# Kernel optimization log

Hardware: AMD Instinct MI355X
Metric: run time of the kernel (lower is better)

The kernel has to match this reference:

```python
import jax, jax.numpy as jnp
import numpy as np

N_NODES = 50000
N_EDGES = 800000
D = 128
N_REL = 237


def _layer(x, W_I, W_O, rel, b, src, dst):
    # messages over real edges: compose (sub) then project
    msg = (x[src] - rel[edge_safe(dst, None) if False else None] if False else (x[src] - rel_gather)) if False else None
    # (see clean version below)
    raise NotImplementedError


def compgcn_layer(x, W_I, W_O, rel, b, src, dst, etype):
    n = x.shape[0]
    # real edges: gather, compose (sub), project, scatter-add at dst
    msg = (x[src] - rel[etype]) @ W_I.T            # [E, out]
    aggr = jax.ops.segment_sum(msg, dst, num_segments=n)
    # self loops (added with edge_type 0): each node contributes to itself
    self_msg = (x - rel[0]) @ W_I.T                # [N, out]
    # update: aggregated messages + W_O(x) + bias
    return aggr + self_msg + x @ W_O.T + b


def setup_inputs() -> dict:
    key = jax.random.key(0)
    ks = jax.random.split(key, 12)
    x = jax.random.normal(ks[0], (N_NODES, D), dtype=jnp.float32)
    edge_index = jax.random.randint(ks[1], (2, N_EDGES), 0, N_NODES, dtype=jnp.int32)
    edge_type = jax.random.randint(ks[2], (N_EDGES,), 0, N_REL, dtype=jnp.int32)
    def xavier(k, shape):
        bound = float(np.sqrt(6.0 / (shape[0] + shape[1])))
        return jax.random.uniform(k, shape, jnp.float32, -bound, bound)
    return {
        "x": x,
        "edge_index": edge_index,
        "edge_type": edge_type,
        "W_I1": xavier(ks[3], (D, D)), "W_O1": xavier(ks[4], (D, D)),
        "rel1": xavier(ks[5], (N_REL, D)), "b1": jnp.zeros((D,), jnp.float32),
        "W_I2": xavier(ks[6], (D, D)), "W_O2": xavier(ks[7], (D, D)),
        "rel2": xavier(ks[8], (N_REL, D)), "b2": jnp.zeros((D,), jnp.float32),
    }


def reference(x, edge_index, edge_type, W_I1, W_O1, rel1, b1, W_I2, W_O2, rel2, b2):
    src, dst = edge_index[0], edge_index[1]
    h = compgcn_layer(x, W_I1, W_O1, rel1, b1, src, dst, edge_type)
    h = jax.nn.relu(h)  # dropout inactive in eval
    out = compgcn_layer(h, W_I2, W_O2, rel2, b2, src, dst, edge_type)
    return out
```

## Files before the change

### kernel.cpp

```cpp
#include <hip/hip_runtime.h>

#define D 128
#define CAP 3072

typedef __attribute__((ext_vector_type(8))) short short8;
typedef __attribute__((ext_vector_type(4))) float f32x4;

__device__ __forceinline__ float blo(unsigned w) { return __uint_as_float(w << 16); }
__device__ __forceinline__ float bhi(unsigned w) { return __uint_as_float(w & 0xFFFF0000u); }
__device__ __forceinline__ unsigned bpack(float a, float b) {
    unsigned ua = __float_as_uint(a), ub = __float_as_uint(b);
    ua += 0x7FFFu + ((ua >> 16) & 1u);
    ub += 0x7FFFu + ((ub >> 16) & 1u);
    return (ua >> 16) | (ub & 0xFFFF0000u);
}

__global__ __launch_bounds__(256) void setup_mega(
    const float* __restrict__ x,
    const int* __restrict__ srcA, const int* __restrict__ dstA,
    const int* __restrict__ etA,
    const float* __restrict__ WI1, const float* __restrict__ WO1,
    const float* __restrict__ WI2, const float* __restrict__ WO2,
    const float* __restrict__ rel1, const float* __restrict__ rel2,
    const float* __restrict__ b1, const float* __restrict__ b2,
    unsigned* __restrict__ A1,
    unsigned* __restrict__ Wt1, unsigned* __restrict__ Wt2,
    float* __restrict__ c1, float* __restrict__ c2,
    unsigned* __restrict__ rb1, unsigned* __restrict__ rb2,
    int* __restrict__ coarseCnt, unsigned* __restrict__ bulk,
    int N, int E, int relHalf, int nCoarse) {
    int tid = threadIdx.x;
    int bx = blockIdx.x;
    const int B1B = (E + 1023) / 1024;

    if (bx < B1B) {
        __shared__ unsigned pay[1024];
        __shared__ unsigned short ck[1024];
        __shared__ int hist[400];
        __shared__ int base[400];
        int e0 = bx * 1024;
        int cnt = E - e0; if (cnt > 1024) cnt = 1024;
        for (int i = tid; i < nCoarse; i += 256) hist[i] = 0;
        __syncthreads();
        for (int i = tid; i < cnt; i += 256) {
            int e = e0 + i;
            int d = dstA[e];
            pay[i] = (unsigned)srcA[e] | ((unsigned)etA[e] << 17) | ((unsigned)(d & 127) << 25);
            int c = d >> 7;
            ck[i] = (unsigned short)c;
            atomicAdd(&hist[c], 1);
        }
        __syncthreads();
        for (int i = tid; i < nCoarse; i += 256) {
            int h = hist[i];
            base[i] = (h > 0) ? (i * CAP + atomicAdd(&coarseCnt[i], h)) : 0;
            hist[i] = 0;
        }
        __syncthreads();
        for (int i = tid; i < cnt; i += 256) {
            int c = ck[i];
            int pos = base[c] + atomicAdd(&hist[c], 1);
            bulk[pos] = pay[i];
        }
        return;
    }
    bx -= B1B;
    const int CB = (N * 32 + 255) / 256;
    if (bx < CB) {
        int idx = bx * 256 + tid;
        if (idx < N * 32) {
            int n = idx >> 5, q = idx & 31;
            float4 v = ((const float4*)x)[idx];
            uint2 o;
            o.x = bpack(v.x, v.y);
            o.y = bpack(v.z, v.w);
            *(uint2*)(A1 + (size_t)n * 128 + 64 + q * 2) = o;
        }
        return;
    }
    bx -= CB;
    if (bx < 128) {
        int layer = bx >> 6;
        const float* WI = layer ? WI2 : WI1;
        const float* WO = layer ? WO2 : WO1;
        unsigned* Wt = layer ? Wt2 : Wt1;
        int idx = (bx & 63) * 256 + tid;
        int j = idx >> 7;
        int kk = idx & 127;
        int k0 = kk * 2;
        float a, b;
        if (k0 < D) {
            a = WI[j * D + k0];
            b = WI[j * D + k0 + 1];
        } else {
            int kx = k0 - D;
            a = WI[j * D + kx]     + WO[j * D + kx];
            b = WI[j * D + kx + 1] + WO[j * D + kx + 1];
        }
        Wt[idx] = bpack(a, b);
        return;
    }
    bx -= 128;
    if (bx == 0) {
        int layer = tid >> 7;
        int j = tid & (D - 1);
        const float* WI = layer ? WI2 : WI1;
        const float* b  = layer ? b2  : b1;
        const float* rl = layer ? rel2 : rel1;
        float s = b[j];
        for (int k = 0; k < D; ++k) s = fmaf(-WI[j * D + k], rl[k], s);
        (layer ? c2 : c1)[j] = s;
        return;
    }
    bx -= 1;
    {
        int idx = bx * 256 + tid;
        if (idx < 2 * relHalf) {
            const float* src = (idx < relHalf) ? rel1 : rel2;
            unsigned* dst = (idx < relHalf) ? rb1 : rb2;
            int k = (idx < relHalf) ? idx : idx - relHalf;
            float4 v = ((const float4*)src)[k];
            uint2 o;
            o.x = bpack(v.x, v.y);
            o.y = bpack(v.z, v.w);
            *(uint2*)(dst + (size_t)k * 2) = o;
        }
    }
}

__global__ __launch_bounds__(512) void scan_coarse(const int* __restrict__ coarseCnt,
                                                   int* __restrict__ coarseBase,
                                                   int nCoarse, int E) {
    __shared__ int arr[512];
    int tid = threadIdx.x;
    int c = (tid < nCoarse) ? coarseCnt[tid] : 0;
    arr[tid] = c;
    __syncthreads();
    for (int off = 1; off < 512; off <<= 1) {
        int v = (tid >= off) ? arr[tid - off] : 0;
        __syncthreads();
        arr[tid] += v;
        __syncthreads();
    }
    if (tid < nCoarse) coarseBase[tid] = arr[tid] - c;
    if (tid == nCoarse) coarseBase[tid] = E;
}

__global__ __launch_bounds__(256) void bucket2(const unsigned* __restrict__ bulk,
                                               const int* __restrict__ coarseCnt,
                                               const int* __restrict__ coarseBase,
                                               int* __restrict__ row_ptr,
                                               int* __restrict__ col,
                                               int N, int E, int nCoarse) {
    __shared__ unsigned pay[CAP];
    __shared__ int hist[128];
    __shared__ int cur[128];
    int c = blockIdx.x;
    int tid = threadIdx.x;
    int cnt = coarseCnt[c];
    int cb  = coarseBase[c];
    const unsigned* seg = bulk + (size_t)c * CAP;
    if (tid < 128) hist[tid] = 0;
    __syncthreads();
    for (int i = tid; i < cnt; i += 256) {
        unsigned v = seg[i];
        pay[i] = v;
        atomicAdd(&hist[v >> 25], 1);
    }
    __syncthreads();
    int f = tid;
    int myCnt = (f < 128) ? hist[f] : 0;
    for (int off = 1; off < 128; off <<= 1) {
        int v = (f < 128 && f >= off) ? hist[f - off] : 0;
        __syncthreads();
        if (f < 128) hist[f] += v;
        __syncthreads();
    }
    if (f < 128) {
        int excl = hist[f] - myCnt;
        int d = (c << 7) + f;
        if (d < N) row_ptr[d] = cb + excl;
        cur[f] = cb + excl;
    }
    if (c == nCoarse - 1 && tid == 0) row_ptr[N] = E;
    __syncthreads();
    for (int i = tid; i < cnt; i += 256) {
        unsigned v = pay[i];
        int pos = atomicAdd(&cur[v >> 25], 1);
        col[pos] = (int)(v & 0x1FFFFFFu);
    }
}

__global__ __launch_bounds__(256) void gather_kernel(const unsigned* __restrict__ Asrc,
                                                     const int* __restrict__ col,
                                                     const int* __restrict__ row_ptr,
                                                     const unsigned* __restrict__ relb,
                                                     unsigned* __restrict__ Adst, int N) {
    int n = blockIdx.x * 8 + (threadIdx.x >> 5);
    if (n >= N) return;
    int lane = threadIdx.x & 31;
    int beg = row_ptr[n];
    int end = row_ptr[n + 1];
    float4 s = make_float4(0.f, 0.f, 0.f, 0.f);
    int e = beg;
    for (; e + 11 < end; e += 12) {
        uint2 u[12], r[12];
#pragma unroll
        for (int t = 0; t < 12; ++t) {
            int c = col[e + t];
            u[t] = *(const uint2*)(Asrc + (size_t)(c & 0x1FFFF) * 128 + 64 + 2 * lane);
            r[t] = *(const uint2*)(relb + (size_t)(c >> 17) * 64 + 2 * lane);
        }
#pragma unroll
        for (int t = 0; t < 12; ++t) {
            s.x += blo(u[t].x) - blo(r[t].x);
            s.y += bhi(u[t].x) - bhi(r[t].x);
            s.z += blo(u[t].y) - blo(r[t].y);
            s.w += bhi(u[t].y) - bhi(r[t].y);
        }
    }
    for (; e + 3 < end; e += 4) {
        uint2 u[4], r[4];
#pragma unroll
        for (int t = 0; t < 4; ++t) {
            int c = col[e + t];
            u[t] = *(const uint2*)(Asrc + (size_t)(c & 0x1FFFF) * 128 + 64 + 2 * lane);
            r[t] = *(const uint2*)(relb + (size_t)(c >> 17) * 64 + 2 * lane);
        }
#pragma unroll
        for (int t = 0; t < 4; ++t) {
            s.x += blo(u[t].x) - blo(r[t].x);
            s.y += bhi(u[t].x) - bhi(r[t].x);
            s.z += blo(u[t].y) - blo(r[t].y);
            s.w += bhi(u[t].y) - bhi(r[t].y);
        }
    }
    for (; e < end; ++e) {
        int c = col[e];
        uint2 u = *(const uint2*)(Asrc + (size_t)(c & 0x1FFFF) * 128 + 64 + 2 * lane);
        uint2 r = *(const uint2*)(relb + (size_t)(c >> 17) * 64 + 2 * lane);
        s.x += blo(u.x) - blo(r.x);
        s.y += bhi(u.x) - bhi(r.x);
        s.z += blo(u.y) - blo(r.y);
        s.w += bhi(u.y) - bhi(r.y);
    }
    uint2 o;
    o.x = bpack(s.x, s.y);
    o.y = bpack(s.z, s.w);
    *(uint2*)(Adst + (size_t)n * 128 + 2 * lane) = o;
}

__global__ __launch_bounds__(256) void node_mfma(
    const unsigned* A,
    const unsigned* __restrict__ Wt,
    const float* __restrict__ cvec,
    float* outf,
    unsigned* __restrict__ outb,
    int do_relu, int N) {
    __shared__ unsigned WtS[128 * 32];
    __shared__ unsigned AS[128 * 32];
    int tid = threadIdx.x;
    int w = tid >> 6;
    int lane = tid & 63;
    int m = lane & 15;
    int quad = lane >> 4;
    int nbase = blockIdx.x * 128;

    f32x4 acc[2][8];
#pragma unroll
    for (int nt = 0; nt < 2; ++nt)
#pragma unroll
        for (int t = 0; t < 8; ++t) acc[nt][t] = (f32x4)(0.f);

    for (int kc = 0; kc < 4; ++kc) {
        for (int i = tid; i < 1024; i += 256) {
            int j = i >> 3, q = i & 7;
            uint4 v = ((const uint4*)Wt)[j * 32 + kc * 8 + q];
            *(uint4*)&WtS[j * 32 + 4 * (q ^ (j & 7))] = v;
        }
        for (int i = tid; i < 1024; i += 256) {
            int n = i >> 3, q = i & 7;
            int gn = nbase + n;
            uint4 v = make_uint4(0u, 0u, 0u, 0u);
            if (gn < N) v = ((const uint4*)A)[(size_t)gn * 32 + kc * 8 + q];
            *(uint4*)&AS[n * 32 + 4 * (q ^ (n & 7))] = v;
        }
        __syncthreads();

#pragma unroll
        for (int s = 0; s < 2; ++s) {
            int g = s * 4 + quad;
            int r0 = w * 32 + m;
            int r1 = r0 + 16;
            short8 b0 = *(const short8*)&AS[r0 * 32 + 4 * (g ^ (r0 & 7))];
            short8 b1 = *(const short8*)&AS[r1 * 32 + 4 * (g ^ (r1 & 7))];
#pragma unroll
            for (int t = 0; t < 8; ++t) {
                int jr = t * 16 + m;
                short8 a = *(const short8*)&WtS[jr * 32 + 4 * (g ^ (jr & 7))];
                acc[0][t] = __builtin_amdgcn_mfma_f32_16x16x32_bf16(a, b0, acc[0][t], 0, 0, 0);
                acc[1][t] = __builtin_amdgcn_mfma_f32_16x16x32_bf16(a, b1, acc[1][t], 0, 0, 0);
            }
        }
        __syncthreads();
    }

#pragma unroll
    for (int nt = 0; nt < 2; ++nt) {
        int node = nbase + w * 32 + nt * 16 + m;
        if (node < N) {
#pragma unroll
            for (int t = 0; t < 8; ++t) {
                float4 cv = ((const float4*)cvec)[t * 4 + quad];
                f32x4 a = acc[nt][t];
                float v0 = a[0] + cv.x;
                float v1 = a[1] + cv.y;
                float v2 = a[2] + cv.z;
                float v3 = a[3] + cv.w;
                if (do_relu) {
                    v0 = fmaxf(v0, 0.f); v1 = fmaxf(v1, 0.f);
                    v2 = fmaxf(v2, 0.f); v3 = fmaxf(v3, 0.f);
                }
                if (outf) {
                    ((float4*)outf)[(size_t)node * 32 + t * 4 + quad] =
                        make_float4(v0, v1, v2, v3);
                } else {
                    uint2 o;
                    o.x = bpack(v0, v1);
                    o.y = bpack(v2, v3);
                    ((uint2*)(outb + (size_t)node * 128))[32 + t * 4 + quad] = o;
                }
            }
        }
    }
}

extern "C" void kernel_launch(void* const* d_in, const int* in_sizes, int n_in,
                              void* d_out, int out_size, void* d_ws, size_t ws_size,
                              hipStream_t stream) {
    const float* x    = (const float*)d_in[0];
    const int*   ei   = (const int*)d_in[1];
    const int*   et   = (const int*)d_in[2];
    const float* WI1  = (const float*)d_in[3];
    const float* WO1  = (const float*)d_in[4];
    const float* rel1 = (const float*)d_in[5];
    const float* b1   = (const float*)d_in[6];
    const float* WI2  = (const float*)d_in[7];
    const float* WO2  = (const float*)d_in[8];
    const float* rel2 = (const float*)d_in[9];
    const float* b2   = (const float*)d_in[10];

    const int E = in_sizes[2];
    const int N = in_sizes[0] / D;
    const int* src = ei;
    const int* dst = ei + E;
    const int nCoarse = (N + 127) / 128;

    unsigned* wsu  = (unsigned*)d_ws;
    unsigned* A1   = wsu;
    unsigned* Wt1  = A1 + (size_t)N * 128;
    unsigned* Wt2  = Wt1 + 16384;
    float*    cvec1 = (float*)(Wt2 + 16384);
    float*    cvec2 = cvec1 + D;
    unsigned* rb1  = (unsigned*)(cvec2 + D);
    unsigned* rb2  = rb1 + 237 * 64;
    int*      coarseCnt  = (int*)(rb2 + 237 * 64);
    int*      coarseBase = coarseCnt + 512;
    int*      row_ptr    = coarseBase + 512;
    int*      col        = row_ptr + N + 4;
    unsigned* bulk       = (unsigned*)(col + E);

    unsigned* A2 = (unsigned*)d_out;

    const int relHalf = 237 * 32;
    const int B1B = (E + 1023) / 1024;
    const int CB = (N * 32 + 255) / 256;
    const int RB = (2 * relHalf + 255) / 256;

    hipMemsetAsync(coarseCnt, 0, 512 * sizeof(int), stream);
    setup_mega<<<B1B + CB + 128 + 1 + RB, 256, 0, stream>>>(
        x, src, dst, et, WI1, WO1, WI2, WO2, rel1, rel2, b1, b2,
        A1, Wt1, Wt2, cvec1, cvec2, rb1, rb2,
        coarseCnt, bulk, N, E, relHalf, nCoarse);

    scan_coarse<<<1, 512, 0, stream>>>(coarseCnt, coarseBase, nCoarse, E);
    bucket2<<<nCoarse, 256, 0, stream>>>(bulk, coarseCnt, coarseBase,
                                         row_ptr, col, N, E, nCoarse);

    const int gather_blocks = (N + 7) / 8;
    const int node_blocks = (N + 127) / 128;

    gather_kernel<<<gather_blocks, 256, 0, stream>>>(A1, col, row_ptr, rb1, A1, N);
    node_mfma<<<node_blocks, 256, 0, stream>>>(A1, Wt1, cvec1,
                                               (float*)nullptr, A2, 1, N);

    gather_kernel<<<gather_blocks, 256, 0, stream>>>(A2, col, row_ptr, rb2, A2, N);
    node_mfma<<<node_blocks, 256, 0, stream>>>(A2, Wt2, cvec2,
                                               (float*)d_out, (unsigned*)nullptr, 0, N);
}
```

Measured before the change: 268.2 us.

## Restructure gather to wave-per-node with 16-byte loads across four edge groups

The gather kernel now assigns one 64-lane wave per node instead of 32 lanes. Each group of 16 lanes handles a different edge using 16-byte loads. Column indices are loaded cooperatively, one per lane, and broadcast with shuffles. Partial sums are reduced across the four groups with xor-shuffles before the bf16 pack and store. This aims to widen memory transactions and raise the number of independent edge loads in flight, at the cost of cross-lane reduction overhead and some idle lanes on low-degree nodes.

```diff
diff --git a/kernel.cpp b/kernel.cpp
--- a/kernel.cpp
+++ b/kernel.cpp
@@ -196,58 +196,85 @@
                                                      const int* __restrict__ row_ptr,
                                                      const unsigned* __restrict__ relb,
                                                      unsigned* __restrict__ Adst, int N) {
-    int n = blockIdx.x * 8 + (threadIdx.x >> 5);
+    int n = blockIdx.x * 4 + (threadIdx.x >> 6);
     if (n >= N) return;
-    int lane = threadIdx.x & 31;
+    int lane = threadIdx.x & 63;
+    int g = lane >> 4;
+    int h = lane & 15;
     int beg = row_ptr[n];
     int end = row_ptr[n + 1];
-    float4 s = make_float4(0.f, 0.f, 0.f, 0.f);
-    int e = beg;
-    for (; e + 11 < end; e += 12) {
-        uint2 u[12], r[12];
-#pragma unroll
-        for (int t = 0; t < 12; ++t) {
-            int c = col[e + t];
-            u[t] = *(const uint2*)(Asrc + (size_t)(c & 0x1FFFF) * 128 + 64 + 2 * lane);
-            r[t] = *(const uint2*)(relb + (size_t)(c >> 17) * 64 + 2 * lane);
-        }
-#pragma unroll
-        for (int t = 0; t < 12; ++t) {
-            s.x += blo(u[t].x) - blo(r[t].x);
-            s.y += bhi(u[t].x) - bhi(r[t].x);
-            s.z += blo(u[t].y) - blo(r[t].y);
-            s.w += bhi(u[t].y) - bhi(r[t].y);
-        }
-    }
-    for (; e + 3 < end; e += 4) {
-        uint2 u[4], r[4];
-#pragma unroll
-        for (int t = 0; t < 4; ++t) {
-            int c = col[e + t];
-            u[t] = *(const uint2*)(Asrc + (size_t)(c & 0x1FFFF) * 128 + 64 + 2 * lane);
-            r[t] = *(const uint2*)(relb + (size_t)(c >> 17) * 64 + 2 * lane);
-        }
-#pragma unroll
-        for (int t = 0; t < 4; ++t) {
-            s.x += blo(u[t].x) - blo(r[t].x);
-            s.y += bhi(u[t].x) - bhi(r[t].x);
-            s.z += blo(u[t].y) - blo(r[t].y);
-            s.w += bhi(u[t].y) - bhi(r[t].y);
-        }
-    }
-    for (; e < end; ++e) {
-        int c = col[e];
-        uint2 u = *(const uint2*)(Asrc + (size_t)(c & 0x1FFFF) * 128 + 64 + 2 * lane);
-        uint2 r = *(const uint2*)(relb + (size_t)(c >> 17) * 64 + 2 * lane);
-        s.x += blo(u.x) - blo(r.x);
-        s.y += bhi(u.x) - bhi(r.x);
-        s.z += blo(u.y) - blo(r.y);
-        s.w += bhi(u.y) - bhi(r.y);
-    }
-    uint2 o;
-    o.x = bpack(s.x, s.y);
-    o.y = bpack(s.z, s.w);
-    *(uint2*)(Adst + (size_t)n * 128 + 2 * lane) = o;
+    float s[8];
+#pragma unroll
+    for (int j = 0; j < 8; ++j) s[j] = 0.f;
+
+    for (int base = beg; base < end; base += 64) {
+        int ci = base + lane;
+        unsigned cv = (unsigned)col[(ci < end) ? ci : beg];
+        int m = end - base; if (m > 64) m = 64;
+        int e = 0;
+        for (; e + 16 <= m; e += 16) {
+            uint4 u[4], r[4];
+#pragma unroll
+            for (int t = 0; t < 4; ++t) {
+                unsigned c = (unsigned)__shfl((int)cv, e + 4 * t + g, 64);
+                u[t] = ((const uint4*)(Asrc + (size_t)(c & 0x1FFFFu) * 128 + 64))[h];
+                r[t] = ((const uint4*)(relb + (size_t)(c >> 17) * 64))[h];
+            }
+#pragma unroll
+            for (int t = 0; t < 4; ++t) {
+                s[0] += blo(u[t].x) - blo(r[t].x);
+                s[1] += bhi(u[t].x) - bhi(r[t].x);
+                s[2] += blo(u[t].y) - blo(r[t].y);
+                s[3] += bhi(u[t].y) - bhi(r[t].y);
+                s[4] += blo(u[t].z) - blo(r[t].z);
+                s[5] += bhi(u[t].z) - bhi(r[t].z);
+                s[6] += blo(u[t].w) - blo(r[t].w);
+                s[7] += bhi(u[t].w) - bhi(r[t].w);
+            }
+        }
+        for (; e + 4 <= m; e += 4) {
+            unsigned c = (unsigned)__shfl((int)cv, e + g, 64);
+            uint4 u = ((const uint4*)(Asrc + (size_t)(c & 0x1FFFFu) * 128 + 64))[h];
+            uint4 r = ((const uint4*)(relb + (size_t)(c >> 17) * 64))[h];
+            s[0] += blo(u.x) - blo(r.x);
+            s[1] += bhi(u.x) - bhi(r.x);
+            s[2] += blo(u.y) - blo(r.y);
+            s[3] += bhi(u.y) - bhi(r.y);
+            s[4] += blo(u.z) - blo(r.z);
+            s[5] += bhi(u.z) - bhi(r.z);
+            s[6] += blo(u.w) - blo(r.w);
+            s[7] += bhi(u.w) - bhi(r.w);
+        }
+        if (e < m) {
+            int idx = e + g;
+            unsigned c = (unsigned)__shfl((int)cv, (idx < m) ? idx : 0, 64);
+            if (idx < m) {
+                uint4 u = ((const uint4*)(Asrc + (size_t)(c & 0x1FFFFu) * 128 + 64))[h];
+                uint4 r = ((const uint4*)(relb + (size_t)(c >> 17) * 64))[h];
+                s[0] += blo(u.x) - blo(r.x);
+                s[1] += bhi(u.x) - bhi(r.x);
+                s[2] += blo(u.y) - blo(r.y);
+                s[3] += bhi(u.y) - bhi(r.y);
+                s[4] += blo(u.z) - blo(r.z);
+                s[5] += bhi(u.z) - bhi(r.z);
+                s[6] += blo(u.w) - blo(r.w);
+                s[7] += bhi(u.w) - bhi(r.w);
+            }
+        }
+    }
+#pragma unroll
+    for (int j = 0; j < 8; ++j) {
+        s[j] += __shfl_xor(s[j], 16, 64);
+        s[j] += __shfl_xor(s[j], 32, 64);
+    }
+    if (g == 0) {
+        uint4 o;
+        o.x = bpack(s[0], s[1]);
+        o.y = bpack(s[2], s[3]);
+        o.z = bpack(s[4], s[5]);
+        o.w = bpack(s[6], s[7]);
+        ((uint4*)(Adst + (size_t)n * 128))[h] = o;
+    }
 }
 
 __global__ __launch_bounds__(256) void node_mfma(
@@ -387,7 +414,7 @@
     bucket2<<<nCoarse, 256, 0, stream>>>(bulk, coarseCnt, coarseBase,
                                          row_ptr, col, N, E, nCoarse);
 
-    const int gather_blocks = (N + 7) / 8;
+    const int gather_blocks = (N + 3) / 4;
     const int node_blocks = (N + 127) / 128;
 
     gather_kernel<<<gather_blocks, 256, 0, stream>>>(A1, col, row_ptr, rb1, A1, N);
```

After: 247.0 us. -7.9%, faster.
